# Optimization experiments

Hardware: AMD Instinct MI355X
Metric: run time of the kernel (lower is better)

## Reference

```python
import jax, jax.numpy as jnp
import numpy as np

FP8_MAX = 448.0   # float8_e4m3fn max magnitude
BS = 128          # quantization block size


def setup_inputs() -> dict:
    key = jax.random.key(0)
    k1, k2 = jax.random.split(key)
    M, K, N = 4096, 4096, 16384
    x = jax.random.normal(k1, (M, K), jnp.float32)
    # Build an FP8 block-quantized weight the way load() expects it:
    # weight holds fp8-representable values, weight_scale_inv is per 128x128 block.
    w = jax.random.normal(k2, (N, K), jnp.float32) * 0.02
    wb = w.reshape(N // BS, BS, K // BS, BS)
    amax = jnp.max(jnp.abs(wb), axis=(1, 3))            # [N/BS, K/BS]
    weight_scale_inv = amax / FP8_MAX                    # fp32 block scales
    wq = (wb / weight_scale_inv[:, None, :, None]).astype(jnp.float8_e4m3fn)
    weight = wq.astype(jnp.float32).reshape(N, K)        # fp8 values held in fp32
    return {"x": x, "weight": weight, "weight_scale_inv": weight_scale_inv}


def reference(x, weight, weight_scale_inv):
    M, K = x.shape
    N = weight.shape[0]
    # --- act_quant: per-(row, 128-block) FP8 quantization of activations ---
    xb = x.reshape(M, K // BS, BS)
    s_x = jnp.max(jnp.abs(xb), axis=-1) / FP8_MAX        # [M, K/BS] fp32 scales
    xq = (xb / s_x[..., None]).astype(jnp.float8_e4m3fn) # simulate fp8 rounding
    # --- fp8_gemm: scaled GEMM with inline dequantization ---
    x_dq = (xq.astype(jnp.float32) * s_x[..., None]).reshape(M, K)
    w_dq = (weight.reshape(N // BS, BS, K // BS, BS)
            * weight_scale_inv[:, None, :, None]).reshape(N, K)
    # y[m, n] = sum_k x_dq[m, k] * w_dq[n, k]
    return jnp.einsum('mk,nk->mn', x_dq, w_dq)
```

## Files before the change

### kernel.cpp

```cpp
#include <hip/hip_runtime.h>
#include <stdint.h>

#define FP8_MAX 448.0f
#define BSQ 128
#define TM 128
#define TN 128
#define NKB 32

typedef int   i32x4  __attribute__((ext_vector_type(4)));
typedef int   i32x8  __attribute__((ext_vector_type(8)));
typedef float f32x4v __attribute__((ext_vector_type(4)));
typedef float f32x16 __attribute__((ext_vector_type(16)));

typedef const __attribute__((address_space(1))) uint8_t* gptr_t;
typedef __attribute__((address_space(3))) uint8_t* lptr_t;

__device__ __forceinline__ int hsw(int row) { return (row ^ (row >> 3)) & 7; }

__global__ void act_quant_kernel(const float* __restrict__ x,
                                 uint8_t* __restrict__ xq,
                                 float* __restrict__ sx,
                                 int M, int K) {
    int gid  = blockIdx.x * blockDim.x + threadIdx.x;
    int wave = gid >> 6;
    int lane = threadIdx.x & 63;
    int nkb  = K / BSQ;
    int row  = wave / nkb;
    int kb   = wave - row * nkb;
    if (row >= M) return;

    const float2 v = *(const float2*)(x + (size_t)row * K + kb * BSQ + lane * 2);
    float am = fmaxf(fabsf(v.x), fabsf(v.y));
#pragma unroll
    for (int off = 32; off >= 1; off >>= 1)
        am = fmaxf(am, __shfl_xor(am, off));

    float s = am / FP8_MAX;
    if (lane == 0) sx[(size_t)row * nkb + kb] = s;

    float q0 = (am > 0.f) ? v.x / s : 0.f;
    float q1 = (am > 0.f) ? v.y / s : 0.f;
    int packed = __builtin_amdgcn_cvt_pk_fp8_f32(q0, q1, 0, false);
    *(uint16_t*)(xq + (size_t)row * K + kb * BSQ + lane * 2) = (uint16_t)(packed & 0xffff);
}

__global__ void weight_quant_kernel(const float* __restrict__ w,
                                    uint8_t* __restrict__ wq, size_t n) {
    size_t i = ((size_t)blockIdx.x * blockDim.x + threadIdx.x) * 4;
    if (i >= n) return;
    float4 v = *(const float4*)(w + i);
    int lo = __builtin_amdgcn_cvt_pk_fp8_f32(v.x, v.y, 0, false);
    int hi = __builtin_amdgcn_cvt_pk_fp8_f32(v.z, v.w, 0, false);
    *(uint32_t*)(wq + i) = (uint32_t)((lo & 0xffff) | (hi << 16));
}

__global__ __launch_bounds__(256, 2)
void fp8_gemm_mx(const uint8_t* __restrict__ Aq,
                 const uint8_t* __restrict__ Bq,
                 const float*  __restrict__ sxg,
                 const float*  __restrict__ swg,
                 float* __restrict__ out,
                 int M, int N, int K) {
    __shared__ uint8_t As[TM * BSQ];
    __shared__ uint8_t Bs[TN * BSQ];
    __shared__ float   sxs[NKB * TM];

    const int tid  = threadIdx.x;
    const int lane = tid & 63;
    const int wid  = tid >> 6;
    const int brow = blockIdx.y * TM;
    const int bcol = blockIdx.x * TN;
    const int nkb  = K / BSQ;
    const int nb   = bcol >> 7;

    for (int i = tid; i < NKB * TM; i += 256) {
        int row = i >> 5, kb = i & 31;
        sxs[kb * TM + row] = sxg[(size_t)(brow + row) * nkb + kb]
                           * swg[(size_t)nb * nkb + kb];
    }

    const int wy = wid >> 1, wx = wid & 1;
    const int fl = lane & 31, hi = lane >> 5;

    const f32x16 zz = {0.f,0.f,0.f,0.f, 0.f,0.f,0.f,0.f,
                       0.f,0.f,0.f,0.f, 0.f,0.f,0.f,0.f};
    f32x16 acc[2][2];
#pragma unroll
    for (int i = 0; i < 2; ++i)
#pragma unroll
        for (int j = 0; j < 2; ++j) acc[i][j] = zz;

    for (int kb = 0; kb < nkb; ++kb) {
        __syncthreads();
#pragma unroll
        for (int r = 0; r < 4; ++r) {
            int slot = r * 256 + tid;
            int row  = slot >> 3;
            int g    = (slot & 7) ^ hsw(row);
            const uint8_t* gA = Aq + (size_t)(brow + row) * K + kb * BSQ + g * 16;
            const uint8_t* gB = Bq + (size_t)(bcol + row) * K + kb * BSQ + g * 16;
            __builtin_amdgcn_global_load_lds((gptr_t)gA, (lptr_t)(As + (slot & ~63) * 16), 16, 0, 0);
            __builtin_amdgcn_global_load_lds((gptr_t)gB, (lptr_t)(Bs + (slot & ~63) * 16), 16, 0, 0);
        }
        __syncthreads();

        i32x8 bfr[2][2];
#pragma unroll
        for (int fn = 0; fn < 2; ++fn) {
            int row = wx * 64 + fn * 32 + fl;
            int hh  = hsw(row);
            const uint8_t* base = Bs + row * BSQ;
#pragma unroll
            for (int kh = 0; kh < 2; ++kh) {
                int g0 = kh * 4 + hi * 2;
                i32x4 lo = *(const i32x4*)(base + (((g0    ) ^ hh) << 4));
                i32x4 h4 = *(const i32x4*)(base + (((g0 + 1) ^ hh) << 4));
                bfr[fn][kh] = (i32x8){lo.x, lo.y, lo.z, lo.w, h4.x, h4.y, h4.z, h4.w};
            }
        }

#pragma unroll
        for (int fm = 0; fm < 2; ++fm) {
            int arow = wy * 64 + fm * 32 + fl;
            int hh   = hsw(arow);
            const uint8_t* abase = As + arow * BSQ;
            i32x8 afr[2];
#pragma unroll
            for (int kh = 0; kh < 2; ++kh) {
                int g0 = kh * 4 + hi * 2;
                i32x4 lo = *(const i32x4*)(abase + (((g0    ) ^ hh) << 4));
                i32x4 h4 = *(const i32x4*)(abase + (((g0 + 1) ^ hh) << 4));
                afr[kh] = (i32x8){lo.x, lo.y, lo.z, lo.w, h4.x, h4.y, h4.z, h4.w};
            }
            f32x4v s4[4];
#pragma unroll
            for (int q = 0; q < 4; ++q)
                s4[q] = *(const f32x4v*)&sxs[kb * TM + wy * 64 + fm * 32 + q * 8 + hi * 4];

#pragma unroll
            for (int fn = 0; fn < 2; ++fn) {
                f32x16 p = __builtin_amdgcn_mfma_scale_f32_32x32x64_f8f6f4(
                    afr[0], bfr[fn][0], zz, 0, 0, 0, 127, 0, 127);
                p = __builtin_amdgcn_mfma_scale_f32_32x32x64_f8f6f4(
                    afr[1], bfr[fn][1], p, 0, 0, 0, 127, 0, 127);
#pragma unroll
                for (int q = 0; q < 4; ++q)
#pragma unroll
                    for (int j = 0; j < 4; ++j)
                        acc[fm][fn][q * 4 + j] += p[q * 4 + j] * s4[q][j];
            }
        }
    }

#pragma unroll
    for (int fm = 0; fm < 2; ++fm)
#pragma unroll
        for (int fn = 0; fn < 2; ++fn)
#pragma unroll
            for (int q = 0; q < 4; ++q)
#pragma unroll
                for (int j = 0; j < 4; ++j) {
                    int row = brow + wy * 64 + fm * 32 + q * 8 + hi * 4 + j;
                    int col = bcol + wx * 64 + fn * 32 + fl;
                    out[(size_t)row * N + col] = acc[fm][fn][q * 4 + j];
                }
}

extern "C" void kernel_launch(void* const* d_in, const int* in_sizes, int n_in,
                              void* d_out, int out_size, void* d_ws, size_t ws_size,
                              hipStream_t stream) {
    const float* x   = (const float*)d_in[0];
    const float* w   = (const float*)d_in[1];
    const float* wsi = (const float*)d_in[2];
    float* out = (float*)d_out;

    const int K = 4096;
    const int M = in_sizes[0] / K;
    const int N = in_sizes[1] / K;

    uint8_t* xq = (uint8_t*)d_ws;
    uint8_t* wq = xq + (size_t)M * K;
    float*   sx = (float*)(wq + (size_t)N * K);

    int waves = M * (K / BSQ);
    act_quant_kernel<<<dim3(waves / 4), dim3(256), 0, stream>>>(x, xq, sx, M, K);

    size_t wn = (size_t)N * K;
    weight_quant_kernel<<<dim3((unsigned)(wn / 4 / 256)), dim3(256), 0, stream>>>(w, wq, wn);

    dim3 grid(N / TN, M / TM);
    fp8_gemm_mx<<<grid, dim3(256), 0, stream>>>(xq, wq, sx, wsi, out, M, N, K);
}
```

Before: 511.0 us.

## Enlarge GEMM tiles to 256x256 with double-buffered LDS prefetch and XCD swizzle

```diff
diff --git a/kernel.cpp b/kernel.cpp
--- a/kernel.cpp
+++ b/kernel.cpp
@@ -3,8 +3,9 @@
 
 #define FP8_MAX 448.0f
 #define BSQ 128
-#define TM 128
-#define TN 128
+#define BM 256
+#define BN 256
+#define BK 128
 #define NKB 32
 
 typedef int   i32x4  __attribute__((ext_vector_type(4)));
@@ -19,7 +20,7 @@
 
 __global__ void act_quant_kernel(const float* __restrict__ x,
                                  uint8_t* __restrict__ xq,
-                                 float* __restrict__ sx,
+                                 float* __restrict__ sxT,
                                  int M, int K) {
     int gid  = blockIdx.x * blockDim.x + threadIdx.x;
     int wave = gid >> 6;
@@ -36,7 +37,7 @@
         am = fmaxf(am, __shfl_xor(am, off));
 
     float s = am / FP8_MAX;
-    if (lane == 0) sx[(size_t)row * nkb + kb] = s;
+    if (lane == 0) sxT[(size_t)kb * M + row] = s;
 
     float q0 = (am > 0.f) ? v.x / s : 0.f;
     float q1 = (am > 0.f) ? v.y / s : 0.f;
@@ -54,62 +55,83 @@
     *(uint32_t*)(wq + i) = (uint32_t)((lo & 0xffff) | (hi << 16));
 }
 
-__global__ __launch_bounds__(256, 2)
-void fp8_gemm_mx(const uint8_t* __restrict__ Aq,
-                 const uint8_t* __restrict__ Bq,
-                 const float*  __restrict__ sxg,
-                 const float*  __restrict__ swg,
-                 float* __restrict__ out,
-                 int M, int N, int K) {
-    __shared__ uint8_t As[TM * BSQ];
-    __shared__ uint8_t Bs[TN * BSQ];
-    __shared__ float   sxs[NKB * TM];
+__global__ __launch_bounds__(512, 2)
+void fp8_gemm_mx8(const uint8_t* __restrict__ Aq,
+                  const uint8_t* __restrict__ Bq,
+                  const float*  __restrict__ sxT,
+                  const float*  __restrict__ swg,
+                  float* __restrict__ out,
+                  int M, int N, int K) {
+    __shared__ uint8_t As[2][BM * BK];
+    __shared__ uint8_t Bs[2][BN * BK];
+    __shared__ float   sxs[2][BM];
 
     const int tid  = threadIdx.x;
     const int lane = tid & 63;
     const int wid  = tid >> 6;
-    const int brow = blockIdx.y * TM;
-    const int bcol = blockIdx.x * TN;
-    const int nkb  = K / BSQ;
-    const int nb   = bcol >> 7;
-
-    for (int i = tid; i < NKB * TM; i += 256) {
-        int row = i >> 5, kb = i & 31;
-        sxs[kb * TM + row] = sxg[(size_t)(brow + row) * nkb + kb]
-                           * swg[(size_t)nb * nkb + kb];
-    }
-
-    const int wy = wid >> 1, wx = wid & 1;
-    const int fl = lane & 31, hi = lane >> 5;
+    const int wy   = wid >> 2;
+    const int wx   = wid & 3;
+    const int fl   = lane & 31;
+    const int hi   = lane >> 5;
+
+    const int nwg = gridDim.x;
+    const int cpx = nwg >> 3;
+    const int swz = (blockIdx.x & 7) * cpx + (blockIdx.x >> 3);
+    const int nbx = N / BN;
+    const int brow = (swz / nbx) * BM;
+    const int bcol = (swz % nbx) * BN;
+
+    auto STAGE = [&](int buf, int kb) {
+#pragma unroll
+        for (int r = 0; r < 4; ++r) {
+            int slot = r * 512 + tid;
+            int row  = slot >> 3;
+            int g    = (slot & 7) ^ hsw(row);
+            const uint8_t* gA = Aq + (size_t)(brow + row) * K + kb * BK + g * 16;
+            __builtin_amdgcn_global_load_lds((gptr_t)gA,
+                (lptr_t)(As[buf] + (slot & ~63) * 16), 16, 0, 0);
+        }
+#pragma unroll
+        for (int r = 0; r < 4; ++r) {
+            int slot = r * 512 + tid;
+            int row  = slot >> 3;
+            int g    = (slot & 7) ^ hsw(row);
+            const uint8_t* gB = Bq + (size_t)(bcol + row) * K + kb * BK + g * 16;
+            __builtin_amdgcn_global_load_lds((gptr_t)gB,
+                (lptr_t)(Bs[buf] + (slot & ~63) * 16), 16, 0, 0);
+        }
+        if (wid < 4) {
+            const float* gs = sxT + (size_t)kb * M + brow + wid * 64 + lane;
+            __builtin_amdgcn_global_load_lds((gptr_t)(const uint8_t*)gs,
+                (lptr_t)(sxs[buf] + wid * 64), 4, 0, 0);
+        }
+    };
 
     const f32x16 zz = {0.f,0.f,0.f,0.f, 0.f,0.f,0.f,0.f,
                        0.f,0.f,0.f,0.f, 0.f,0.f,0.f,0.f};
-    f32x16 acc[2][2];
-#pragma unroll
-    for (int i = 0; i < 2; ++i)
+    f32x16 acc[4][2];
+#pragma unroll
+    for (int i = 0; i < 4; ++i)
 #pragma unroll
         for (int j = 0; j < 2; ++j) acc[i][j] = zz;
 
-    for (int kb = 0; kb < nkb; ++kb) {
-        __syncthreads();
-#pragma unroll
-        for (int r = 0; r < 4; ++r) {
-            int slot = r * 256 + tid;
-            int row  = slot >> 3;
-            int g    = (slot & 7) ^ hsw(row);
-            const uint8_t* gA = Aq + (size_t)(brow + row) * K + kb * BSQ + g * 16;
-            const uint8_t* gB = Bq + (size_t)(bcol + row) * K + kb * BSQ + g * 16;
-            __builtin_amdgcn_global_load_lds((gptr_t)gA, (lptr_t)(As + (slot & ~63) * 16), 16, 0, 0);
-            __builtin_amdgcn_global_load_lds((gptr_t)gB, (lptr_t)(Bs + (slot & ~63) * 16), 16, 0, 0);
-        }
-        __syncthreads();
+    STAGE(0, 0);
+    asm volatile("s_waitcnt vmcnt(0)" ::: "memory");
+    __syncthreads();
+
+    for (int kb = 0; kb < NKB; ++kb) {
+        const int c = kb & 1;
+        const uint8_t* Ab = As[c];
+        const uint8_t* Bb = Bs[c];
+        const float*   Sb = sxs[c];
+        const float sw = swg[(size_t)((bcol >> 7) + (wx >> 1)) * NKB + kb];
 
         i32x8 bfr[2][2];
 #pragma unroll
         for (int fn = 0; fn < 2; ++fn) {
             int row = wx * 64 + fn * 32 + fl;
             int hh  = hsw(row);
-            const uint8_t* base = Bs + row * BSQ;
+            const uint8_t* base = Bb + row * BK;
 #pragma unroll
             for (int kh = 0; kh < 2; ++kh) {
                 int g0 = kh * 4 + hi * 2;
@@ -120,10 +142,12 @@
         }
 
 #pragma unroll
-        for (int fm = 0; fm < 2; ++fm) {
-            int arow = wy * 64 + fm * 32 + fl;
+        for (int fm = 0; fm < 4; ++fm) {
+            __builtin_amdgcn_s_barrier();
+
+            int arow = wy * 128 + fm * 32 + fl;
             int hh   = hsw(arow);
-            const uint8_t* abase = As + arow * BSQ;
+            const uint8_t* abase = Ab + arow * BK;
             i32x8 afr[2];
 #pragma unroll
             for (int kh = 0; kh < 2; ++kh) {
@@ -134,33 +158,46 @@
             }
             f32x4v s4[4];
 #pragma unroll
+            for (int q = 0; q < 4; ++q) {
+                s4[q] = *(const f32x4v*)&Sb[wy * 128 + fm * 32 + q * 8 + hi * 4];
+                s4[q] *= sw;
+            }
+
+            if (fm == 0 && kb + 1 < NKB) STAGE(c ^ 1, kb + 1);
+
+            __builtin_amdgcn_s_setprio(1);
+            f32x16 p0 = __builtin_amdgcn_mfma_scale_f32_32x32x64_f8f6f4(
+                afr[0], bfr[0][0], zz, 0, 0, 0, 127, 0, 127);
+            p0 = __builtin_amdgcn_mfma_scale_f32_32x32x64_f8f6f4(
+                afr[1], bfr[0][1], p0, 0, 0, 0, 127, 0, 127);
+            f32x16 p1 = __builtin_amdgcn_mfma_scale_f32_32x32x64_f8f6f4(
+                afr[0], bfr[1][0], zz, 0, 0, 0, 127, 0, 127);
+            p1 = __builtin_amdgcn_mfma_scale_f32_32x32x64_f8f6f4(
+                afr[1], bfr[1][1], p1, 0, 0, 0, 127, 0, 127);
+            __builtin_amdgcn_s_setprio(0);
+
+#pragma unroll
             for (int q = 0; q < 4; ++q)
-                s4[q] = *(const f32x4v*)&sxs[kb * TM + wy * 64 + fm * 32 + q * 8 + hi * 4];
-
-#pragma unroll
-            for (int fn = 0; fn < 2; ++fn) {
-                f32x16 p = __builtin_amdgcn_mfma_scale_f32_32x32x64_f8f6f4(
-                    afr[0], bfr[fn][0], zz, 0, 0, 0, 127, 0, 127);
-                p = __builtin_amdgcn_mfma_scale_f32_32x32x64_f8f6f4(
-                    afr[1], bfr[fn][1], p, 0, 0, 0, 127, 0, 127);
-#pragma unroll
-                for (int q = 0; q < 4; ++q)
-#pragma unroll
-                    for (int j = 0; j < 4; ++j)
-                        acc[fm][fn][q * 4 + j] += p[q * 4 + j] * s4[q][j];
-            }
-        }
+#pragma unroll
+                for (int j = 0; j < 4; ++j) {
+                    acc[fm][0][q * 4 + j] += p0[q * 4 + j] * s4[q][j];
+                    acc[fm][1][q * 4 + j] += p1[q * 4 + j] * s4[q][j];
+                }
+        }
+
+        asm volatile("s_waitcnt vmcnt(0)" ::: "memory");
+        __builtin_amdgcn_s_barrier();
     }
 
 #pragma unroll
-    for (int fm = 0; fm < 2; ++fm)
+    for (int fm = 0; fm < 4; ++fm)
 #pragma unroll
         for (int fn = 0; fn < 2; ++fn)
 #pragma unroll
             for (int q = 0; q < 4; ++q)
 #pragma unroll
                 for (int j = 0; j < 4; ++j) {
-                    int row = brow + wy * 64 + fm * 32 + q * 8 + hi * 4 + j;
+                    int row = brow + wy * 128 + fm * 32 + q * 8 + hi * 4 + j;
                     int col = bcol + wx * 64 + fn * 32 + fl;
                     out[(size_t)row * N + col] = acc[fm][fn][q * 4 + j];
                 }
@@ -178,16 +215,16 @@
     const int M = in_sizes[0] / K;
     const int N = in_sizes[1] / K;
 
-    uint8_t* xq = (uint8_t*)d_ws;
-    uint8_t* wq = xq + (size_t)M * K;
-    float*   sx = (float*)(wq + (size_t)N * K);
+    uint8_t* xq  = (uint8_t*)d_ws;
+    uint8_t* wq  = xq + (size_t)M * K;
+    float*   sxT = (float*)(wq + (size_t)N * K);
 
     int waves = M * (K / BSQ);
-    act_quant_kernel<<<dim3(waves / 4), dim3(256), 0, stream>>>(x, xq, sx, M, K);
+    act_quant_kernel<<<dim3(waves / 4), dim3(256), 0, stream>>>(x, xq, sxT, M, K);
 
     size_t wn = (size_t)N * K;
     weight_quant_kernel<<<dim3((unsigned)(wn / 4 / 256)), dim3(256), 0, stream>>>(w, wq, wn);
 
-    dim3 grid(N / TN, M / TM);
-    fp8_gemm_mx<<<grid, dim3(256), 0, stream>>>(xq, wq, sx, wsi, out, M, N, K);
-}
+    dim3 grid((N / BN) * (M / BM));
+    fp8_gemm_mx8<<<grid, dim3(512), 0, stream>>>(xq, wq, sxT, wsi, out, M, N, K);
+}
```

After: 592.3 us. 15.9% more time.

## Double-buffer GEMM LDS tiles and stream transposed activation scales per k-block

Applied to the files above, without the earlier changes.

```diff
diff --git a/kernel.cpp b/kernel.cpp
--- a/kernel.cpp
+++ b/kernel.cpp
@@ -19,7 +19,7 @@
 
 __global__ void act_quant_kernel(const float* __restrict__ x,
                                  uint8_t* __restrict__ xq,
-                                 float* __restrict__ sx,
+                                 float* __restrict__ sxT,
                                  int M, int K) {
     int gid  = blockIdx.x * blockDim.x + threadIdx.x;
     int wave = gid >> 6;
@@ -36,7 +36,7 @@
         am = fmaxf(am, __shfl_xor(am, off));
 
     float s = am / FP8_MAX;
-    if (lane == 0) sx[(size_t)row * nkb + kb] = s;
+    if (lane == 0) sxT[(size_t)kb * M + row] = s;
 
     float q0 = (am > 0.f) ? v.x / s : 0.f;
     float q1 = (am > 0.f) ? v.y / s : 0.f;
@@ -57,41 +57,25 @@
 __global__ __launch_bounds__(256, 2)
 void fp8_gemm_mx(const uint8_t* __restrict__ Aq,
                  const uint8_t* __restrict__ Bq,
-                 const float*  __restrict__ sxg,
+                 const float*  __restrict__ sxT,
                  const float*  __restrict__ swg,
                  float* __restrict__ out,
                  int M, int N, int K) {
-    __shared__ uint8_t As[TM * BSQ];
-    __shared__ uint8_t Bs[TN * BSQ];
-    __shared__ float   sxs[NKB * TM];
+    __shared__ uint8_t As[2][TM * BSQ];
+    __shared__ uint8_t Bs[2][TN * BSQ];
+    __shared__ float   sxs[2][TM];
 
     const int tid  = threadIdx.x;
     const int lane = tid & 63;
     const int wid  = tid >> 6;
     const int brow = blockIdx.y * TM;
     const int bcol = blockIdx.x * TN;
-    const int nkb  = K / BSQ;
     const int nb   = bcol >> 7;
-
-    for (int i = tid; i < NKB * TM; i += 256) {
-        int row = i >> 5, kb = i & 31;
-        sxs[kb * TM + row] = sxg[(size_t)(brow + row) * nkb + kb]
-                           * swg[(size_t)nb * nkb + kb];
-    }
 
     const int wy = wid >> 1, wx = wid & 1;
     const int fl = lane & 31, hi = lane >> 5;
 
-    const f32x16 zz = {0.f,0.f,0.f,0.f, 0.f,0.f,0.f,0.f,
-                       0.f,0.f,0.f,0.f, 0.f,0.f,0.f,0.f};
-    f32x16 acc[2][2];
-#pragma unroll
-    for (int i = 0; i < 2; ++i)
-#pragma unroll
-        for (int j = 0; j < 2; ++j) acc[i][j] = zz;
-
-    for (int kb = 0; kb < nkb; ++kb) {
-        __syncthreads();
+    auto STAGE = [&](int buf, int kb) {
 #pragma unroll
         for (int r = 0; r < 4; ++r) {
             int slot = r * 256 + tid;
@@ -99,17 +83,45 @@
             int g    = (slot & 7) ^ hsw(row);
             const uint8_t* gA = Aq + (size_t)(brow + row) * K + kb * BSQ + g * 16;
             const uint8_t* gB = Bq + (size_t)(bcol + row) * K + kb * BSQ + g * 16;
-            __builtin_amdgcn_global_load_lds((gptr_t)gA, (lptr_t)(As + (slot & ~63) * 16), 16, 0, 0);
-            __builtin_amdgcn_global_load_lds((gptr_t)gB, (lptr_t)(Bs + (slot & ~63) * 16), 16, 0, 0);
-        }
-        __syncthreads();
+            __builtin_amdgcn_global_load_lds((gptr_t)gA,
+                (lptr_t)(As[buf] + (slot & ~63) * 16), 16, 0, 0);
+            __builtin_amdgcn_global_load_lds((gptr_t)gB,
+                (lptr_t)(Bs[buf] + (slot & ~63) * 16), 16, 0, 0);
+        }
+        if (wid < 2) {
+            const float* gs = sxT + (size_t)kb * M + brow + wid * 64 + lane;
+            __builtin_amdgcn_global_load_lds((gptr_t)(const uint8_t*)gs,
+                (lptr_t)(sxs[buf] + wid * 64), 4, 0, 0);
+        }
+    };
+
+    const f32x16 zz = {0.f,0.f,0.f,0.f, 0.f,0.f,0.f,0.f,
+                       0.f,0.f,0.f,0.f, 0.f,0.f,0.f,0.f};
+    f32x16 acc[2][2];
+#pragma unroll
+    for (int i = 0; i < 2; ++i)
+#pragma unroll
+        for (int j = 0; j < 2; ++j) acc[i][j] = zz;
+
+    STAGE(0, 0);
+    __syncthreads();
+
+    for (int kb = 0; kb < NKB; ++kb) {
+        const int cur = kb & 1;
+        const uint8_t* Ab = As[cur];
+        const uint8_t* Bb = Bs[cur];
+        const float*   Sb = sxs[cur];
+
+        if (kb + 1 < NKB) STAGE(cur ^ 1, kb + 1);
+
+        const float sw = swg[(size_t)nb * NKB + kb];
 
         i32x8 bfr[2][2];
 #pragma unroll
         for (int fn = 0; fn < 2; ++fn) {
             int row = wx * 64 + fn * 32 + fl;
             int hh  = hsw(row);
-            const uint8_t* base = Bs + row * BSQ;
+            const uint8_t* base = Bb + row * BSQ;
 #pragma unroll
             for (int kh = 0; kh < 2; ++kh) {
                 int g0 = kh * 4 + hi * 2;
@@ -123,7 +135,7 @@
         for (int fm = 0; fm < 2; ++fm) {
             int arow = wy * 64 + fm * 32 + fl;
             int hh   = hsw(arow);
-            const uint8_t* abase = As + arow * BSQ;
+            const uint8_t* abase = Ab + arow * BSQ;
             i32x8 afr[2];
 #pragma unroll
             for (int kh = 0; kh < 2; ++kh) {
@@ -134,8 +146,10 @@
             }
             f32x4v s4[4];
 #pragma unroll
-            for (int q = 0; q < 4; ++q)
-                s4[q] = *(const f32x4v*)&sxs[kb * TM + wy * 64 + fm * 32 + q * 8 + hi * 4];
+            for (int q = 0; q < 4; ++q) {
+                s4[q] = *(const f32x4v*)&Sb[wy * 64 + fm * 32 + q * 8 + hi * 4];
+                s4[q] *= sw;
+            }
 
 #pragma unroll
             for (int fn = 0; fn < 2; ++fn) {
@@ -150,6 +164,8 @@
                         acc[fm][fn][q * 4 + j] += p[q * 4 + j] * s4[q][j];
             }
         }
+
+        __syncthreads();
     }
 
 #pragma unroll
@@ -162,7 +178,8 @@
                 for (int j = 0; j < 4; ++j) {
                     int row = brow + wy * 64 + fm * 32 + q * 8 + hi * 4 + j;
                     int col = bcol + wx * 64 + fn * 32 + fl;
-                    out[(size_t)row * N + col] = acc[fm][fn][q * 4 + j];
+                    __builtin_nontemporal_store(acc[fm][fn][q * 4 + j],
+                                                &out[(size_t)row * N + col]);
                 }
 }
 
@@ -178,16 +195,16 @@
     const int M = in_sizes[0] / K;
     const int N = in_sizes[1] / K;
 
-    uint8_t* xq = (uint8_t*)d_ws;
-    uint8_t* wq = xq + (size_t)M * K;
-    float*   sx = (float*)(wq + (size_t)N * K);
+    uint8_t* xq  = (uint8_t*)d_ws;
+    uint8_t* wq  = xq + (size_t)M * K;
+    float*   sxT = (float*)(wq + (size_t)N * K);
 
     int waves = M * (K / BSQ);
-    act_quant_kernel<<<dim3(waves / 4), dim3(256), 0, stream>>>(x, xq, sx, M, K);
+    act_quant_kernel<<<dim3(waves / 4), dim3(256), 0, stream>>>(x, xq, sxT, M, K);
 
     size_t wn = (size_t)N * K;
     weight_quant_kernel<<<dim3((unsigned)(wn / 4 / 256)), dim3(256), 0, stream>>>(w, wq, wn);
 
     dim3 grid(N / TN, M / TM);
-    fp8_gemm_mx<<<grid, dim3(256), 0, stream>>>(xq, wq, sx, wsi, out, M, N, K);
-}
+    fp8_gemm_mx<<<grid, dim3(256), 0, stream>>>(xq, wq, sxT, wsi, out, M, N, K);
+}
```

Result: faster. 458.4 us (-10.3%).
